# Kernel tuning notes

Measured on AMD Instinct MI355X. Metric: run time of the kernel, lower is better.

## Reference

```python
import jax, jax.numpy as jnp
import numpy as np

B, T, D = 8, 1024, 1024
H, G = 16, 4            # num_heads, query_groups
HD = D // H             # head_dim = 64
REP = H // G            # heads_per_group
EPS = 1e-10
NEG = -1e9


def setup_inputs() -> dict:
    key = jax.random.key(0)
    k1, k2, k3 = jax.random.split(key, 3)
    x = jax.random.normal(k1, (B, T, D), dtype=jnp.float32)
    w_qkv = jax.random.normal(k2, (D, H * HD + 2 * G * HD), dtype=jnp.float32) * (D ** -0.5)
    w_o = jax.random.normal(k3, (D, D), dtype=jnp.float32) * (D ** -0.5)
    padding_mask = jnp.ones((B, T), dtype=bool)
    return {"x": x, "w_qkv": w_qkv, "w_o": w_o, "padding_mask": padding_mask}


def _l2_norm(t):
    # qk_norm_type=2: L2 normalize over head_dim
    return t / (jnp.sqrt(jnp.sum(t * t, axis=-1, keepdims=True)) + EPS)


def reference(x, w_qkv, w_o, padding_mask):
    # fused QKV projection: [B,T,D] @ [D, H*HD + 2*G*HD]
    qkv = x @ w_qkv
    q, k, v = jnp.split(qkv, [H * HD, H * HD + G * HD], axis=-1)
    q = q.reshape(B, T, H, HD)
    k = k.reshape(B, T, G, HD)
    v = v.reshape(B, T, G, HD)
    # QK normalization (L2 over head_dim)
    q = _l2_norm(q)
    k = _l2_norm(k)
    # GQA: expand KV heads (repeat_interleave along head dim)
    k = jnp.repeat(k, REP, axis=2)  # [B,T,H,HD]
    v = jnp.repeat(v, REP, axis=2)
    # to [B,H,T,HD]
    q = q.transpose(0, 2, 1, 3)
    k = k.transpose(0, 2, 1, 3)
    v = v.transpose(0, 2, 1, 3)
    # causal + padding mask, True = attend
    causal = jnp.tril(jnp.ones((T, T), dtype=bool))  # [T_q, T_k]
    valid = padding_mask[:, None, :, None] & padding_mask[:, None, None, :] & causal[None, None]
    scale = HD ** -0.5  # SDPA default scale
    scores = jnp.einsum('bhqd,bhkd->bhqk', q, k) * scale
    scores = jnp.where(valid, scores, NEG)
    attn = jax.nn.softmax(scores, axis=-1)
    out = jnp.einsum('bhqk,bhkd->bhqd', attn, v)  # [B,H,T,HD]
    out = out.transpose(0, 2, 1, 3).reshape(B, T, D)
    return out @ w_o
```

## Files before the change

kernel.cpp:

```cpp
#include <hip/hip_runtime.h>
#include <hip/hip_bf16.h>

typedef __attribute__((ext_vector_type(8))) short short8;
typedef __attribute__((ext_vector_type(4))) short short4v;
typedef __attribute__((ext_vector_type(4))) float f32x4;

#define B_ 8
#define T_ 1024
#define D_ 1024
#define H_ 16
#define G_ 4
#define HD_ 64
#define QKVW 1536

#define GLOAD16(gp, lp) __builtin_amdgcn_global_load_lds( \
    (const __attribute__((address_space(1))) void*)(gp),  \
    (__attribute__((address_space(3))) void*)(lp), 16, 0, 0)

__device__ __forceinline__ float exp2_fast(float x) {
    return __builtin_amdgcn_exp2f(x);
}

__global__ __launch_bounds__(256) void cvt_f32_bf16(
    const float* __restrict__ in, __hip_bfloat16* __restrict__ out, int n)
{
    int i = (blockIdx.x * 256 + threadIdx.x) * 8;
    if (i >= n) return;
    float4 a = *reinterpret_cast<const float4*>(in + i);
    float4 b = *reinterpret_cast<const float4*>(in + i + 4);
    union { short8 s; __hip_bfloat16 h[8]; } u;
    u.h[0] = __float2bfloat16(a.x); u.h[1] = __float2bfloat16(a.y);
    u.h[2] = __float2bfloat16(a.z); u.h[3] = __float2bfloat16(a.w);
    u.h[4] = __float2bfloat16(b.x); u.h[5] = __float2bfloat16(b.y);
    u.h[6] = __float2bfloat16(b.z); u.h[7] = __float2bfloat16(b.w);
    *reinterpret_cast<short8*>(out + i) = u.s;
}

__global__ __launch_bounds__(256) void cvt_transpose(
    const float* __restrict__ in, __hip_bfloat16* __restrict__ outT, int K, int N)
{
    __shared__ float tile[32][33];
    const int k0 = blockIdx.y * 32, n0 = blockIdx.x * 32;
    const int r = threadIdx.x >> 5, c = threadIdx.x & 31;
    #pragma unroll
    for (int i = 0; i < 4; ++i)
        tile[r + i * 8][c] = in[(size_t)(k0 + r + i * 8) * N + n0 + c];
    __syncthreads();
    #pragma unroll
    for (int i = 0; i < 4; ++i)
        outT[(size_t)(n0 + r + i * 8) * K + k0 + c] = __float2bfloat16(tile[c][r + i * 8]);
}

__global__ __launch_bounds__(256) void gemm_qkv(
    const __hip_bfloat16* __restrict__ A,
    const __hip_bfloat16* __restrict__ Bt,
    __hip_bfloat16* __restrict__ qkv,
    __hip_bfloat16* __restrict__ vt)
{
    const int M = B_ * T_, K = D_;
    __shared__ __hip_bfloat16 As[2][128 * 32];
    __shared__ __hip_bfloat16 Bs[2][128 * 32];

    const int tid  = threadIdx.x;
    const int lane = tid & 63;
    const int wr   = (tid >> 6) >> 1;
    const int wc   = (tid >> 6) & 1;

    const int rpx = (M >> 7) >> 3;
    const int xcd = blockIdx.x & 7;
    const int lin = blockIdx.x >> 3;
    const int by  = xcd * rpx + (lin % rpx);
    const int bx  = lin / rpx;
    const int m0 = by * 128;
    const int n0 = bx * 128;

    f32x4 acc[4][4] = {};

    const int s0 = tid * 8,          sr0 = s0 >> 5, sc0 = s0 & 31;
    const int s1 = (256 + tid) * 8,  sr1 = s1 >> 5, sc1 = s1 & 31;

    const __hip_bfloat16* Ar0 = A  + (size_t)(m0 + sr0) * K + sc0;
    const __hip_bfloat16* Ar1 = A  + (size_t)(m0 + sr1) * K + sc1;
    const __hip_bfloat16* Br0 = Bt + (size_t)(n0 + sr0) * K + sc0;
    const __hip_bfloat16* Br1 = Bt + (size_t)(n0 + sr1) * K + sc1;

    const int fr = lane & 15;
    const int kf = (lane >> 4) * 8;

    GLOAD16(Ar0, &As[0][s0]);
    GLOAD16(Ar1, &As[0][s1]);
    GLOAD16(Br0, &Bs[0][s0]);
    GLOAD16(Br1, &Bs[0][s1]);
    __syncthreads();

    int cur = 0;
    for (int kk = 0; kk < K; kk += 32) {
        const int nxt = cur ^ 1;
        if (kk + 32 < K) {
            GLOAD16(Ar0 + kk + 32, &As[nxt][s0]);
            GLOAD16(Ar1 + kk + 32, &As[nxt][s1]);
            GLOAD16(Br0 + kk + 32, &Bs[nxt][s0]);
            GLOAD16(Br1 + kk + 32, &Bs[nxt][s1]);
        }
        short8 a[4], b[4];
        #pragma unroll
        for (int m = 0; m < 4; ++m)
            a[m] = *reinterpret_cast<const short8*>(&As[cur][(wr * 64 + m * 16 + fr) * 32 + kf]);
        #pragma unroll
        for (int n = 0; n < 4; ++n)
            b[n] = *reinterpret_cast<const short8*>(&Bs[cur][(wc * 64 + n * 16 + fr) * 32 + kf]);
        #pragma unroll
        for (int m = 0; m < 4; ++m)
            #pragma unroll
            for (int n = 0; n < 4; ++n)
                acc[m][n] = __builtin_amdgcn_mfma_f32_16x16x32_bf16(a[m], b[n], acc[m][n], 0, 0, 0);
        __syncthreads();
        cur = nxt;
    }

    const int rowb  = m0 + wr * 64 + (lane >> 4) * 4;
    const int colb0 = n0 + wc * 64;

    if (n0 < 1280) {
        const float extra = (n0 < 1024) ? 0.18033688f : 1.0f;
        #pragma unroll
        for (int m = 0; m < 4; ++m)
            #pragma unroll
            for (int r = 0; r < 4; ++r) {
                float ss = 0.f;
                #pragma unroll
                for (int n = 0; n < 4; ++n) { float v = acc[m][n][r]; ss += v * v; }
                ss += __shfl_xor(ss, 1, 64);
                ss += __shfl_xor(ss, 2, 64);
                ss += __shfl_xor(ss, 4, 64);
                ss += __shfl_xor(ss, 8, 64);
                float sc = extra / (sqrtf(ss) + 1e-10f);
                const size_t rbase = (size_t)(rowb + m * 16 + r) * QKVW + colb0 + fr;
                #pragma unroll
                for (int n = 0; n < 4; ++n)
                    qkv[rbase + n * 16] = __float2bfloat16(acc[m][n][r] * sc);
            }
    } else {
        #pragma unroll
        for (int m = 0; m < 4; ++m) {
            const int row = rowb + m * 16;
            const int b   = row >> 10;
            const int t0  = row & 1023;
            #pragma unroll
            for (int n = 0; n < 4; ++n) {
                const int cv = colb0 + fr + n * 16 - 1280;
                const int gg = cv >> 6, d = cv & 63;
                union { short4v s; __hip_bfloat16 h[4]; } u;
                u.h[0] = __float2bfloat16(acc[m][n][0]);
                u.h[1] = __float2bfloat16(acc[m][n][1]);
                u.h[2] = __float2bfloat16(acc[m][n][2]);
                u.h[3] = __float2bfloat16(acc[m][n][3]);
                *reinterpret_cast<short4v*>(
                    vt + ((size_t)((b * G_ + gg) * HD_ + d)) * T_ + t0) = u.s;
            }
        }
    }
}

__global__ __launch_bounds__(256) void gemm_tn_f32(
    const __hip_bfloat16* __restrict__ A,
    const __hip_bfloat16* __restrict__ Bt,
    float* __restrict__ C, int M, int N, int K)
{
    __shared__ __hip_bfloat16 As[2][128 * 32];
    __shared__ __hip_bfloat16 Bs[2][128 * 32];

    const int tid  = threadIdx.x;
    const int lane = tid & 63;
    const int wr   = (tid >> 6) >> 1;
    const int wc   = (tid >> 6) & 1;

    const int rpx = (M >> 7) >> 3;
    const int xcd = blockIdx.x & 7;
    const int lin = blockIdx.x >> 3;
    const int by  = xcd * rpx + (lin % rpx);
    const int bx  = lin / rpx;
    const int m0 = by * 128;
    const int n0 = bx * 128;

    f32x4 acc[4][4] = {};

    const int s0 = tid * 8,          sr0 = s0 >> 5, sc0 = s0 & 31;
    const int s1 = (256 + tid) * 8,  sr1 = s1 >> 5, sc1 = s1 & 31;

    const __hip_bfloat16* Ar0 = A  + (size_t)(m0 + sr0) * K + sc0;
    const __hip_bfloat16* Ar1 = A  + (size_t)(m0 + sr1) * K + sc1;
    const __hip_bfloat16* Br0 = Bt + (size_t)(n0 + sr0) * K + sc0;
    const __hip_bfloat16* Br1 = Bt + (size_t)(n0 + sr1) * K + sc1;

    const int fr = lane & 15;
    const int kf = (lane >> 4) * 8;

    GLOAD16(Ar0, &As[0][s0]);
    GLOAD16(Ar1, &As[0][s1]);
    GLOAD16(Br0, &Bs[0][s0]);
    GLOAD16(Br1, &Bs[0][s1]);
    __syncthreads();

    int cur = 0;
    for (int kk = 0; kk < K; kk += 32) {
        const int nxt = cur ^ 1;
        if (kk + 32 < K) {
            GLOAD16(Ar0 + kk + 32, &As[nxt][s0]);
            GLOAD16(Ar1 + kk + 32, &As[nxt][s1]);
            GLOAD16(Br0 + kk + 32, &Bs[nxt][s0]);
            GLOAD16(Br1 + kk + 32, &Bs[nxt][s1]);
        }
        short8 a[4], b[4];
        #pragma unroll
        for (int m = 0; m < 4; ++m)
            a[m] = *reinterpret_cast<const short8*>(&As[cur][(wr * 64 + m * 16 + fr) * 32 + kf]);
        #pragma unroll
        for (int n = 0; n < 4; ++n)
            b[n] = *reinterpret_cast<const short8*>(&Bs[cur][(wc * 64 + n * 16 + fr) * 32 + kf]);
        #pragma unroll
        for (int m = 0; m < 4; ++m)
            #pragma unroll
            for (int n = 0; n < 4; ++n)
                acc[m][n] = __builtin_amdgcn_mfma_f32_16x16x32_bf16(a[m], b[n], acc[m][n], 0, 0, 0);
        __syncthreads();
        cur = nxt;
    }

    const int rowb = m0 + wr * 64 + (lane >> 4) * 4;
    const int colb = n0 + wc * 64 + fr;
    #pragma unroll
    for (int m = 0; m < 4; ++m)
        #pragma unroll
        for (int n = 0; n < 4; ++n)
            #pragma unroll
            for (int r = 0; r < 4; ++r)
                C[(size_t)(rowb + m * 16 + r) * N + colb + n * 16] = acc[m][n][r];
}

__global__ __launch_bounds__(256) void attn_fwd(
    const __hip_bfloat16* __restrict__ qkv,
    const __hip_bfloat16* __restrict__ vt,
    __hip_bfloat16* __restrict__ out)
{
    const int pair = blockIdx.x;
    const int h  = blockIdx.y;
    const int b  = blockIdx.z;
    const int g  = h >> 2;

    const int tid  = threadIdx.x;
    const int lane = tid & 63;
    const int wid  = tid >> 6;

    __shared__ __hip_bfloat16 Ks[2 * 4096];
    __shared__ __hip_bfloat16 Vs[2 * 4096];
    __shared__ __hip_bfloat16 Ps[4 * 16 * 64];

    const int fr  = lane & 15;
    const int kf  = (lane >> 4) * 8;
    const int kb  = kf * 2;
    const int swz = (fr & 7) << 4;

    const int srow = tid >> 3;
    const int scol = ((tid & 7) * 8) ^ ((srow & 7) << 3);

    const size_t kgbase = (size_t)(b * T_) * QKVW + H_ * HD_ + g * HD_ + scol;
    const size_t vgbase = (size_t)((b * G_ + g) * HD_) * T_ + scol;

    char* PsB = (char*)Ps + wid * 2048;

    for (int half = 0; half < 2; ++half) {
        const int qt = half ? (15 - pair) : pair;
        const int q0 = qt * 64;
        const int arow  = q0 + wid * 16 + fr;
        const int rbase = q0 + wid * 16 + (lane >> 4) * 4;

        short8 qfrag0, qfrag1;
        {
            const size_t qbase = ((size_t)(b * T_ + arow)) * QKVW + h * HD_;
            qfrag0 = *reinterpret_cast<const short8*>(qkv + qbase + kf);
            qfrag1 = *reinterpret_cast<const short8*>(qkv + qbase + 32 + kf);
        }

        float lsum[4] = {0.f, 0.f, 0.f, 0.f};
        f32x4 o[4] = {};

        GLOAD16(qkv + kgbase + (size_t)srow * QKVW,        &Ks[tid * 8]);
        GLOAD16(qkv + kgbase + (size_t)(32 + srow) * QKVW, &Ks[2048 + tid * 8]);
        GLOAD16(vt + vgbase + (size_t)srow * T_,           &Vs[tid * 8]);
        GLOAD16(vt + vgbase + (size_t)(32 + srow) * T_,    &Vs[2048 + tid * 8]);
        __syncthreads();

        int cur = 0;
        for (int kt = 0; kt <= qt; ++kt) {
            const bool diag = (kt == qt);
            const int  nb   = (cur ^ 1) * 4096;

            if (!diag) {
                GLOAD16(qkv + kgbase + (size_t)((kt + 1) * 64 + srow) * QKVW,      &Ks[nb + tid * 8]);
                GLOAD16(qkv + kgbase + (size_t)((kt + 1) * 64 + 32 + srow) * QKVW, &Ks[nb + 2048 + tid * 8]);
                GLOAD16(vt + vgbase + (size_t)srow * T_ + (kt + 1) * 64,           &Vs[nb + tid * 8]);
                GLOAD16(vt + vgbase + (size_t)(32 + srow) * T_ + (kt + 1) * 64,    &Vs[nb + 2048 + tid * 8]);
            }

            char* KsB = (char*)(Ks + cur * 4096);
            char* VsB = (char*)(Vs + cur * 4096);

            f32x4 s[4] = {};
            #pragma unroll
            for (int nf = 0; nf < 4; ++nf) {
                const int row = fr + 16 * nf;
                short8 b0 = *reinterpret_cast<const short8*>(KsB + row * 128 + (kb ^ swz));
                short8 b1 = *reinterpret_cast<const short8*>(KsB + row * 128 + ((64 + kb) ^ swz));
                s[nf] = __builtin_amdgcn_mfma_f32_16x16x32_bf16(qfrag0, b0, s[nf], 0, 0, 0);
                s[nf] = __builtin_amdgcn_mfma_f32_16x16x32_bf16(qfrag1, b1, s[nf], 0, 0, 0);
            }

            if (diag) {
                #pragma unroll
                for (int nf = 0; nf < 4; ++nf) {
                    int col = kt * 64 + fr + 16 * nf;
                    #pragma unroll
                    for (int r = 0; r < 4; ++r) {
                        float p = (col <= rbase + r) ? exp2_fast(s[nf][r]) : 0.f;
                        lsum[r] += p;
                        int q = (lane >> 4) * 4 + r;
                        *(__hip_bfloat16*)(PsB + q * 128 +
                            ((2 * (fr + 16 * nf)) ^ ((q & 7) << 4))) = __float2bfloat16(p);
                    }
                }
            } else {
                #pragma unroll
                for (int nf = 0; nf < 4; ++nf)
                    #pragma unroll
                    for (int r = 0; r < 4; ++r) {
                        float p = exp2_fast(s[nf][r]);
                        lsum[r] += p;
                        int q = (lane >> 4) * 4 + r;
                        *(__hip_bfloat16*)(PsB + q * 128 +
                            ((2 * (fr + 16 * nf)) ^ ((q & 7) << 4))) = __float2bfloat16(p);
                    }
            }

            short8 pa0 = *reinterpret_cast<const short8*>(PsB + fr * 128 + (kb ^ swz));
            short8 pa1 = *reinterpret_cast<const short8*>(PsB + fr * 128 + ((64 + kb) ^ swz));
            #pragma unroll
            for (int nf = 0; nf < 4; ++nf) {
                const int row = fr + 16 * nf;
                short8 b0 = *reinterpret_cast<const short8*>(VsB + row * 128 + (kb ^ swz));
                short8 b1 = *reinterpret_cast<const short8*>(VsB + row * 128 + ((64 + kb) ^ swz));
                o[nf] = __builtin_amdgcn_mfma_f32_16x16x32_bf16(pa0, b0, o[nf], 0, 0, 0);
                o[nf] = __builtin_amdgcn_mfma_f32_16x16x32_bf16(pa1, b1, o[nf], 0, 0, 0);
            }
            __syncthreads();
            cur ^= 1;
        }

        float linv[4];
        #pragma unroll
        for (int r = 0; r < 4; ++r) {
            float v = lsum[r];
            v += __shfl_xor(v, 1, 64);
            v += __shfl_xor(v, 2, 64);
            v += __shfl_xor(v, 4, 64);
            v += __shfl_xor(v, 8, 64);
            linv[r] = 1.0f / v;
        }
        #pragma unroll
        for (int nf = 0; nf < 4; ++nf) {
            int col = fr + 16 * nf;
            #pragma unroll
            for (int r = 0; r < 4; ++r) {
                float v = o[nf][r] * linv[r];
                out[((size_t)(b * T_ + rbase + r)) * (H_ * HD_) + h * HD_ + col] =
                    __float2bfloat16(v);
            }
        }
    }
}

extern "C" void kernel_launch(void* const* d_in, const int* in_sizes, int n_in,
                              void* d_out, int out_size, void* d_ws, size_t ws_size,
                              hipStream_t stream) {
    const float* x_f     = (const float*)d_in[0];
    const float* w_qkv_f = (const float*)d_in[1];
    const float* w_o_f   = (const float*)d_in[2];
    float* out = (float*)d_out;

    const int NX  = B_ * T_ * D_;
    const int NWQ = D_ * QKVW;
    const int NWO = D_ * D_;

    __hip_bfloat16* xb    = (__hip_bfloat16*)d_ws;
    __hip_bfloat16* wqkvT = xb + NX;
    __hip_bfloat16* woT   = wqkvT + NWQ;
    __hip_bfloat16* qkv   = woT + NWO;
    __hip_bfloat16* vt    = qkv + (size_t)(B_ * T_) * QKVW;
    __hip_bfloat16* attn_out = xb;

    dim3 blk(256);

    cvt_f32_bf16<<<dim3(NX / 2048), blk, 0, stream>>>(x_f, xb, NX);
    cvt_transpose<<<dim3(QKVW / 32, D_ / 32), blk, 0, stream>>>(w_qkv_f, wqkvT, D_, QKVW);
    cvt_transpose<<<dim3(D_ / 32, D_ / 32), blk, 0, stream>>>(w_o_f, woT, D_, D_);

    gemm_qkv<<<dim3((QKVW / 128) * ((B_ * T_) / 128)), blk, 0, stream>>>(
        xb, wqkvT, qkv, vt);

    attn_fwd<<<dim3(8, H_, B_), blk, 0, stream>>>(qkv, vt, attn_out);

    gemm_tn_f32<<<dim3((D_ / 128) * ((B_ * T_) / 128)), blk, 0, stream>>>(
        attn_out, woT, out, B_ * T_, D_, D_);
}
```

Measured before the change: 130.3 us.

## Fuse x fp32-to-bf16 conversion into QKV GEMM and interleave attention query tiles

Removes the separate x conversion kernel: the QKV GEMM now loads fp32 x into registers, converts it to bf16 and stores it into LDS after the MFMAs, which saves one full pass over x in global memory. The attention kernel processes its two query tiles (pair and 15-pair) together in a single key loop, so each K/V tile is loaded and read from LDS once for both tiles, and the MFMA sections are wrapped in s_setprio. In exchange the GEMM's A-operand loads go through registers instead of direct-to-LDS loads, and the attention kernel needs more registers and twice the P scratch in LDS, which may lower occupancy.

```diff
diff --git a/kernel.cpp b/kernel.cpp
--- a/kernel.cpp
+++ b/kernel.cpp
@@ -21,19 +21,13 @@
     return __builtin_amdgcn_exp2f(x);
 }
 
-__global__ __launch_bounds__(256) void cvt_f32_bf16(
-    const float* __restrict__ in, __hip_bfloat16* __restrict__ out, int n)
-{
-    int i = (blockIdx.x * 256 + threadIdx.x) * 8;
-    if (i >= n) return;
-    float4 a = *reinterpret_cast<const float4*>(in + i);
-    float4 b = *reinterpret_cast<const float4*>(in + i + 4);
+__device__ __forceinline__ short8 pack_bf16x8(float4 a, float4 b) {
     union { short8 s; __hip_bfloat16 h[8]; } u;
     u.h[0] = __float2bfloat16(a.x); u.h[1] = __float2bfloat16(a.y);
     u.h[2] = __float2bfloat16(a.z); u.h[3] = __float2bfloat16(a.w);
     u.h[4] = __float2bfloat16(b.x); u.h[5] = __float2bfloat16(b.y);
     u.h[6] = __float2bfloat16(b.z); u.h[7] = __float2bfloat16(b.w);
-    *reinterpret_cast<short8*>(out + i) = u.s;
+    return u.s;
 }
 
 __global__ __launch_bounds__(256) void cvt_transpose(
@@ -52,7 +46,7 @@
 }
 
 __global__ __launch_bounds__(256) void gemm_qkv(
-    const __hip_bfloat16* __restrict__ A,
+    const float* __restrict__ Af,
     const __hip_bfloat16* __restrict__ Bt,
     __hip_bfloat16* __restrict__ qkv,
     __hip_bfloat16* __restrict__ vt)
@@ -79,41 +73,52 @@
     const int s0 = tid * 8,          sr0 = s0 >> 5, sc0 = s0 & 31;
     const int s1 = (256 + tid) * 8,  sr1 = s1 >> 5, sc1 = s1 & 31;
 
-    const __hip_bfloat16* Ar0 = A  + (size_t)(m0 + sr0) * K + sc0;
-    const __hip_bfloat16* Ar1 = A  + (size_t)(m0 + sr1) * K + sc1;
+    const float* Ar0f = Af + (size_t)(m0 + sr0) * K + sc0;
+    const float* Ar1f = Af + (size_t)(m0 + sr1) * K + sc1;
     const __hip_bfloat16* Br0 = Bt + (size_t)(n0 + sr0) * K + sc0;
     const __hip_bfloat16* Br1 = Bt + (size_t)(n0 + sr1) * K + sc1;
 
     const int fr = lane & 15;
     const int kf = (lane >> 4) * 8;
 
-    GLOAD16(Ar0, &As[0][s0]);
-    GLOAD16(Ar1, &As[0][s1]);
+    float4 a0a = *(const float4*)(Ar0f);
+    float4 a0b = *(const float4*)(Ar0f + 4);
+    float4 a1a = *(const float4*)(Ar1f);
+    float4 a1b = *(const float4*)(Ar1f + 4);
     GLOAD16(Br0, &Bs[0][s0]);
     GLOAD16(Br1, &Bs[0][s1]);
+    *(short8*)&As[0][s0] = pack_bf16x8(a0a, a0b);
+    *(short8*)&As[0][s1] = pack_bf16x8(a1a, a1b);
     __syncthreads();
 
     int cur = 0;
     for (int kk = 0; kk < K; kk += 32) {
         const int nxt = cur ^ 1;
-        if (kk + 32 < K) {
-            GLOAD16(Ar0 + kk + 32, &As[nxt][s0]);
-            GLOAD16(Ar1 + kk + 32, &As[nxt][s1]);
+        const bool more = (kk + 32 < K);
+        if (more) {
+            a0a = *(const float4*)(Ar0f + kk + 32);
+            a0b = *(const float4*)(Ar0f + kk + 36);
+            a1a = *(const float4*)(Ar1f + kk + 32);
+            a1b = *(const float4*)(Ar1f + kk + 36);
             GLOAD16(Br0 + kk + 32, &Bs[nxt][s0]);
             GLOAD16(Br1 + kk + 32, &Bs[nxt][s1]);
         }
         short8 a[4], b[4];
         #pragma unroll
         for (int m = 0; m < 4; ++m)
-            a[m] = *reinterpret_cast<const short8*>(&As[cur][(wr * 64 + m * 16 + fr) * 32 + kf]);
+            a[m] = *(const short8*)(&As[cur][(wr * 64 + m * 16 + fr) * 32 + kf]);
         #pragma unroll
         for (int n = 0; n < 4; ++n)
-            b[n] = *reinterpret_cast<const short8*>(&Bs[cur][(wc * 64 + n * 16 + fr) * 32 + kf]);
+            b[n] = *(const short8*)(&Bs[cur][(wc * 64 + n * 16 + fr) * 32 + kf]);
         #pragma unroll
         for (int m = 0; m < 4; ++m)
             #pragma unroll
             for (int n = 0; n < 4; ++n)
                 acc[m][n] = __builtin_amdgcn_mfma_f32_16x16x32_bf16(a[m], b[n], acc[m][n], 0, 0, 0);
+        if (more) {
+            *(short8*)&As[nxt][s0] = pack_bf16x8(a0a, a0b);
+            *(short8*)&As[nxt][s1] = pack_bf16x8(a1a, a1b);
+        }
         __syncthreads();
         cur = nxt;
     }
@@ -144,7 +149,7 @@
         #pragma unroll
         for (int m = 0; m < 4; ++m) {
             const int row = rowb + m * 16;
-            const int b   = row >> 10;
+            const int bb  = row >> 10;
             const int t0  = row & 1023;
             #pragma unroll
             for (int n = 0; n < 4; ++n) {
@@ -156,7 +161,7 @@
                 u.h[2] = __float2bfloat16(acc[m][n][2]);
                 u.h[3] = __float2bfloat16(acc[m][n][3]);
                 *reinterpret_cast<short4v*>(
-                    vt + ((size_t)((b * G_ + gg) * HD_ + d)) * T_ + t0) = u.s;
+                    vt + ((size_t)((bb * G_ + gg) * HD_ + d)) * T_ + t0) = u.s;
             }
         }
     }
@@ -214,10 +219,10 @@
         short8 a[4], b[4];
         #pragma unroll
         for (int m = 0; m < 4; ++m)
-            a[m] = *reinterpret_cast<const short8*>(&As[cur][(wr * 64 + m * 16 + fr) * 32 + kf]);
+            a[m] = *(const short8*)(&As[cur][(wr * 64 + m * 16 + fr) * 32 + kf]);
         #pragma unroll
         for (int n = 0; n < 4; ++n)
-            b[n] = *reinterpret_cast<const short8*>(&Bs[cur][(wc * 64 + n * 16 + fr) * 32 + kf]);
+            b[n] = *(const short8*)(&Bs[cur][(wc * 64 + n * 16 + fr) * 32 + kf]);
         #pragma unroll
         for (int m = 0; m < 4; ++m)
             #pragma unroll
@@ -254,7 +259,7 @@
 
     __shared__ __hip_bfloat16 Ks[2 * 4096];
     __shared__ __hip_bfloat16 Vs[2 * 4096];
-    __shared__ __hip_bfloat16 Ps[4 * 16 * 64];
+    __shared__ __hip_bfloat16 Ps[4 * 2 * 1024];
 
     const int fr  = lane & 15;
     const int kf  = (lane >> 4) * 8;
@@ -267,63 +272,78 @@
     const size_t kgbase = (size_t)(b * T_) * QKVW + H_ * HD_ + g * HD_ + scol;
     const size_t vgbase = (size_t)((b * G_ + g) * HD_) * T_ + scol;
 
-    char* PsB = (char*)Ps + wid * 2048;
-
-    for (int half = 0; half < 2; ++half) {
-        const int qt = half ? (15 - pair) : pair;
-        const int q0 = qt * 64;
-        const int arow  = q0 + wid * 16 + fr;
-        const int rbase = q0 + wid * 16 + (lane >> 4) * 4;
-
-        short8 qfrag0, qfrag1;
-        {
-            const size_t qbase = ((size_t)(b * T_ + arow)) * QKVW + h * HD_;
-            qfrag0 = *reinterpret_cast<const short8*>(qkv + qbase + kf);
-            qfrag1 = *reinterpret_cast<const short8*>(qkv + qbase + 32 + kf);
-        }
-
-        float lsum[4] = {0.f, 0.f, 0.f, 0.f};
-        f32x4 o[4] = {};
-
-        GLOAD16(qkv + kgbase + (size_t)srow * QKVW,        &Ks[tid * 8]);
-        GLOAD16(qkv + kgbase + (size_t)(32 + srow) * QKVW, &Ks[2048 + tid * 8]);
-        GLOAD16(vt + vgbase + (size_t)srow * T_,           &Vs[tid * 8]);
-        GLOAD16(vt + vgbase + (size_t)(32 + srow) * T_,    &Vs[2048 + tid * 8]);
-        __syncthreads();
-
-        int cur = 0;
-        for (int kt = 0; kt <= qt; ++kt) {
-            const bool diag = (kt == qt);
-            const int  nb   = (cur ^ 1) * 4096;
-
-            if (!diag) {
-                GLOAD16(qkv + kgbase + (size_t)((kt + 1) * 64 + srow) * QKVW,      &Ks[nb + tid * 8]);
-                GLOAD16(qkv + kgbase + (size_t)((kt + 1) * 64 + 32 + srow) * QKVW, &Ks[nb + 2048 + tid * 8]);
-                GLOAD16(vt + vgbase + (size_t)srow * T_ + (kt + 1) * 64,           &Vs[nb + tid * 8]);
-                GLOAD16(vt + vgbase + (size_t)(32 + srow) * T_ + (kt + 1) * 64,    &Vs[nb + 2048 + tid * 8]);
-            }
-
-            char* KsB = (char*)(Ks + cur * 4096);
-            char* VsB = (char*)(Vs + cur * 4096);
-
-            f32x4 s[4] = {};
+    char* PsB = (char*)Ps + wid * 4096;
+
+    const int qtA = pair, qtB = 15 - pair;
+    const int rbaseA = qtA * 64 + wid * 16 + (lane >> 4) * 4;
+    const int rbaseB = qtB * 64 + wid * 16 + (lane >> 4) * 4;
+
+    short8 qA0, qA1, qB0, qB1;
+    {
+        const size_t qa = ((size_t)(b * T_ + qtA * 64 + wid * 16 + fr)) * QKVW + h * HD_;
+        const size_t qb = ((size_t)(b * T_ + qtB * 64 + wid * 16 + fr)) * QKVW + h * HD_;
+        qA0 = *(const short8*)(qkv + qa + kf);
+        qA1 = *(const short8*)(qkv + qa + 32 + kf);
+        qB0 = *(const short8*)(qkv + qb + kf);
+        qB1 = *(const short8*)(qkv + qb + 32 + kf);
+    }
+
+    float lsumA[4] = {0.f, 0.f, 0.f, 0.f}, lsumB[4] = {0.f, 0.f, 0.f, 0.f};
+    f32x4 oA[4] = {}, oB[4] = {};
+
+    GLOAD16(qkv + kgbase + (size_t)srow * QKVW,        &Ks[tid * 8]);
+    GLOAD16(qkv + kgbase + (size_t)(32 + srow) * QKVW, &Ks[2048 + tid * 8]);
+    GLOAD16(vt + vgbase + (size_t)srow * T_,           &Vs[tid * 8]);
+    GLOAD16(vt + vgbase + (size_t)(32 + srow) * T_,    &Vs[2048 + tid * 8]);
+    __syncthreads();
+
+    int cur = 0;
+    for (int kt = 0; kt <= qtB; ++kt) {
+        const bool doA = (kt <= qtA);
+        const int nb = (cur ^ 1) * 4096;
+        if (kt < qtB) {
+            GLOAD16(qkv + kgbase + (size_t)((kt + 1) * 64 + srow) * QKVW,      &Ks[nb + tid * 8]);
+            GLOAD16(qkv + kgbase + (size_t)((kt + 1) * 64 + 32 + srow) * QKVW, &Ks[nb + 2048 + tid * 8]);
+            GLOAD16(vt + vgbase + (size_t)srow * T_ + (kt + 1) * 64,           &Vs[nb + tid * 8]);
+            GLOAD16(vt + vgbase + (size_t)(32 + srow) * T_ + (kt + 1) * 64,    &Vs[nb + 2048 + tid * 8]);
+        }
+
+        char* KsB = (char*)(Ks + cur * 4096);
+        char* VsB = (char*)(Vs + cur * 4096);
+
+        short8 bK0[4], bK1[4];
+        #pragma unroll
+        for (int nf = 0; nf < 4; ++nf) {
+            const int row = fr + 16 * nf;
+            bK0[nf] = *(const short8*)(KsB + row * 128 + (kb ^ swz));
+            bK1[nf] = *(const short8*)(KsB + row * 128 + ((64 + kb) ^ swz));
+        }
+
+        f32x4 sA[4] = {}, sB[4] = {};
+        __builtin_amdgcn_s_setprio(1);
+        if (doA) {
             #pragma unroll
             for (int nf = 0; nf < 4; ++nf) {
-                const int row = fr + 16 * nf;
-                short8 b0 = *reinterpret_cast<const short8*>(KsB + row * 128 + (kb ^ swz));
-                short8 b1 = *reinterpret_cast<const short8*>(KsB + row * 128 + ((64 + kb) ^ swz));
-                s[nf] = __builtin_amdgcn_mfma_f32_16x16x32_bf16(qfrag0, b0, s[nf], 0, 0, 0);
-                s[nf] = __builtin_amdgcn_mfma_f32_16x16x32_bf16(qfrag1, b1, s[nf], 0, 0, 0);
-            }
-
-            if (diag) {
+                sA[nf] = __builtin_amdgcn_mfma_f32_16x16x32_bf16(qA0, bK0[nf], sA[nf], 0, 0, 0);
+                sA[nf] = __builtin_amdgcn_mfma_f32_16x16x32_bf16(qA1, bK1[nf], sA[nf], 0, 0, 0);
+            }
+        }
+        #pragma unroll
+        for (int nf = 0; nf < 4; ++nf) {
+            sB[nf] = __builtin_amdgcn_mfma_f32_16x16x32_bf16(qB0, bK0[nf], sB[nf], 0, 0, 0);
+            sB[nf] = __builtin_amdgcn_mfma_f32_16x16x32_bf16(qB1, bK1[nf], sB[nf], 0, 0, 0);
+        }
+        __builtin_amdgcn_s_setprio(0);
+
+        if (doA) {
+            if (kt == qtA) {
                 #pragma unroll
                 for (int nf = 0; nf < 4; ++nf) {
                     int col = kt * 64 + fr + 16 * nf;
                     #pragma unroll
                     for (int r = 0; r < 4; ++r) {
-                        float p = (col <= rbase + r) ? exp2_fast(s[nf][r]) : 0.f;
-                        lsum[r] += p;
+                        float p = (col <= rbaseA + r) ? exp2_fast(sA[nf][r]) : 0.f;
+                        lsumA[r] += p;
                         int q = (lane >> 4) * 4 + r;
                         *(__hip_bfloat16*)(PsB + q * 128 +
                             ((2 * (fr + 16 * nf)) ^ ((q & 7) << 4))) = __float2bfloat16(p);
@@ -334,47 +354,96 @@
                 for (int nf = 0; nf < 4; ++nf)
                     #pragma unroll
                     for (int r = 0; r < 4; ++r) {
-                        float p = exp2_fast(s[nf][r]);
-                        lsum[r] += p;
+                        float p = exp2_fast(sA[nf][r]);
+                        lsumA[r] += p;
                         int q = (lane >> 4) * 4 + r;
                         *(__hip_bfloat16*)(PsB + q * 128 +
                             ((2 * (fr + 16 * nf)) ^ ((q & 7) << 4))) = __float2bfloat16(p);
                     }
             }
-
-            short8 pa0 = *reinterpret_cast<const short8*>(PsB + fr * 128 + (kb ^ swz));
-            short8 pa1 = *reinterpret_cast<const short8*>(PsB + fr * 128 + ((64 + kb) ^ swz));
+        }
+        if (kt == qtB) {
             #pragma unroll
             for (int nf = 0; nf < 4; ++nf) {
-                const int row = fr + 16 * nf;
-                short8 b0 = *reinterpret_cast<const short8*>(VsB + row * 128 + (kb ^ swz));
-                short8 b1 = *reinterpret_cast<const short8*>(VsB + row * 128 + ((64 + kb) ^ swz));
-                o[nf] = __builtin_amdgcn_mfma_f32_16x16x32_bf16(pa0, b0, o[nf], 0, 0, 0);
-                o[nf] = __builtin_amdgcn_mfma_f32_16x16x32_bf16(pa1, b1, o[nf], 0, 0, 0);
-            }
-            __syncthreads();
-            cur ^= 1;
-        }
-
-        float linv[4];
+                int col = kt * 64 + fr + 16 * nf;
+                #pragma unroll
+                for (int r = 0; r < 4; ++r) {
+                    float p = (col <= rbaseB + r) ? exp2_fast(sB[nf][r]) : 0.f;
+                    lsumB[r] += p;
+                    int q = (lane >> 4) * 4 + r;
+                    *(__hip_bfloat16*)(PsB + 2048 + q * 128 +
+                        ((2 * (fr + 16 * nf)) ^ ((q & 7) << 4))) = __float2bfloat16(p);
+                }
+            }
+        } else {
+            #pragma unroll
+            for (int nf = 0; nf < 4; ++nf)
+                #pragma unroll
+                for (int r = 0; r < 4; ++r) {
+                    float p = exp2_fast(sB[nf][r]);
+                    lsumB[r] += p;
+                    int q = (lane >> 4) * 4 + r;
+                    *(__hip_bfloat16*)(PsB + 2048 + q * 128 +
+                        ((2 * (fr + 16 * nf)) ^ ((q & 7) << 4))) = __float2bfloat16(p);
+                }
+        }
+
+        short8 bV0[4], bV1[4];
+        #pragma unroll
+        for (int nf = 0; nf < 4; ++nf) {
+            const int row = fr + 16 * nf;
+            bV0[nf] = *(const short8*)(VsB + row * 128 + (kb ^ swz));
+            bV1[nf] = *(const short8*)(VsB + row * 128 + ((64 + kb) ^ swz));
+        }
+        __builtin_amdgcn_s_setprio(1);
+        if (doA) {
+            short8 pa0 = *(const short8*)(PsB + fr * 128 + (kb ^ swz));
+            short8 pa1 = *(const short8*)(PsB + fr * 128 + ((64 + kb) ^ swz));
+            #pragma unroll
+            for (int nf = 0; nf < 4; ++nf) {
+                oA[nf] = __builtin_amdgcn_mfma_f32_16x16x32_bf16(pa0, bV0[nf], oA[nf], 0, 0, 0);
+                oA[nf] = __builtin_amdgcn_mfma_f32_16x16x32_bf16(pa1, bV1[nf], oA[nf], 0, 0, 0);
+            }
+        }
+        {
+            short8 pb0 = *(const short8*)(PsB + 2048 + fr * 128 + (kb ^ swz));
+            short8 pb1 = *(const short8*)(PsB + 2048 + fr * 128 + ((64 + kb) ^ swz));
+            #pragma unroll
+            for (int nf = 0; nf < 4; ++nf) {
+                oB[nf] = __builtin_amdgcn_mfma_f32_16x16x32_bf16(pb0, bV0[nf], oB[nf], 0, 0, 0);
+                oB[nf] = __builtin_amdgcn_mfma_f32_16x16x32_bf16(pb1, bV1[nf], oB[nf], 0, 0, 0);
+            }
+        }
+        __builtin_amdgcn_s_setprio(0);
+        __syncthreads();
+        cur ^= 1;
+    }
+
+    float linvA[4], linvB[4];
+    #pragma unroll
+    for (int r = 0; r < 4; ++r) {
+        float va = lsumA[r];
+        va += __shfl_xor(va, 1, 64);
+        va += __shfl_xor(va, 2, 64);
+        va += __shfl_xor(va, 4, 64);
+        va += __shfl_xor(va, 8, 64);
+        linvA[r] = 1.0f / va;
+        float vb = lsumB[r];
+        vb += __shfl_xor(vb, 1, 64);
+        vb += __shfl_xor(vb, 2, 64);
+        vb += __shfl_xor(vb, 4, 64);
+        vb += __shfl_xor(vb, 8, 64);
+        linvB[r] = 1.0f / vb;
+    }
+    #pragma unroll
+    for (int nf = 0; nf < 4; ++nf) {
+        int col = fr + 16 * nf;
         #pragma unroll
         for (int r = 0; r < 4; ++r) {
-            float v = lsum[r];
-            v += __shfl_xor(v, 1, 64);
-            v += __shfl_xor(v, 2, 64);
-            v += __shfl_xor(v, 4, 64);
-            v += __shfl_xor(v, 8, 64);
-            linv[r] = 1.0f / v;
-        }
-        #pragma unroll
-        for (int nf = 0; nf < 4; ++nf) {
-            int col = fr + 16 * nf;
-            #pragma unroll
-            for (int r = 0; r < 4; ++r) {
-                float v = o[nf][r] * linv[r];
-                out[((size_t)(b * T_ + rbase + r)) * (H_ * HD_) + h * HD_ + col] =
-                    __float2bfloat16(v);
-            }
+            out[((size_t)(b * T_ + rbaseA + r)) * (H_ * HD_) + h * HD_ + col] =
+                __float2bfloat16(oA[nf][r] * linvA[r]);
+            out[((size_t)(b * T_ + rbaseB + r)) * (H_ * HD_) + h * HD_ + col] =
+                __float2bfloat16(oB[nf][r] * linvB[r]);
         }
     }
 }
@@ -391,21 +460,19 @@
     const int NWQ = D_ * QKVW;
     const int NWO = D_ * D_;
 
-    __hip_bfloat16* xb    = (__hip_bfloat16*)d_ws;
-    __hip_bfloat16* wqkvT = xb + NX;
+    __hip_bfloat16* attn_out = (__hip_bfloat16*)d_ws;
+    __hip_bfloat16* wqkvT = attn_out + NX;
     __hip_bfloat16* woT   = wqkvT + NWQ;
     __hip_bfloat16* qkv   = woT + NWO;
     __hip_bfloat16* vt    = qkv + (size_t)(B_ * T_) * QKVW;
-    __hip_bfloat16* attn_out = xb;
 
     dim3 blk(256);
 
-    cvt_f32_bf16<<<dim3(NX / 2048), blk, 0, stream>>>(x_f, xb, NX);
     cvt_transpose<<<dim3(QKVW / 32, D_ / 32), blk, 0, stream>>>(w_qkv_f, wqkvT, D_, QKVW);
     cvt_transpose<<<dim3(D_ / 32, D_ / 32), blk, 0, stream>>>(w_o_f, woT, D_, D_);
 
     gemm_qkv<<<dim3((QKVW / 128) * ((B_ * T_) / 128)), blk, 0, stream>>>(
-        xb, wqkvT, qkv, vt);
+        x_f, wqkvT, qkv, vt);
 
     attn_fwd<<<dim3(8, H_, B_), blk, 0, stream>>>(qkv, vt, attn_out);
 
```

Measured after the change: 129.9 us. No clear change (-0.3%).

## Fuse x conversion into QKV GEMM and split attention into per-tile blocks

Applied to the files above, without the earlier changes.

The QKV GEMM now reads fp32 x directly, holds the next tile in registers and converts it to bf16 into LDS after the MFMAs, which removes the separate conversion kernel and its bf16 round trip through memory. The attention kernel no longer pairs query tiles (qt and 15-qt) in one block; it launches 16 blocks per head with one query tile each and adds s_setprio around the MFMA sections. The fused load path adds register pressure and synchronous global loads inside the GEMM loop. The unpaired attention grid gives blocks very different causal workloads and relies on the scheduler to balance them.

```diff
diff --git a/kernel.cpp b/kernel.cpp
--- a/kernel.cpp
+++ b/kernel.cpp
@@ -21,19 +21,13 @@
     return __builtin_amdgcn_exp2f(x);
 }
 
-__global__ __launch_bounds__(256) void cvt_f32_bf16(
-    const float* __restrict__ in, __hip_bfloat16* __restrict__ out, int n)
-{
-    int i = (blockIdx.x * 256 + threadIdx.x) * 8;
-    if (i >= n) return;
-    float4 a = *reinterpret_cast<const float4*>(in + i);
-    float4 b = *reinterpret_cast<const float4*>(in + i + 4);
+__device__ __forceinline__ short8 pack_bf16x8(float4 a, float4 b) {
     union { short8 s; __hip_bfloat16 h[8]; } u;
     u.h[0] = __float2bfloat16(a.x); u.h[1] = __float2bfloat16(a.y);
     u.h[2] = __float2bfloat16(a.z); u.h[3] = __float2bfloat16(a.w);
     u.h[4] = __float2bfloat16(b.x); u.h[5] = __float2bfloat16(b.y);
     u.h[6] = __float2bfloat16(b.z); u.h[7] = __float2bfloat16(b.w);
-    *reinterpret_cast<short8*>(out + i) = u.s;
+    return u.s;
 }
 
 __global__ __launch_bounds__(256) void cvt_transpose(
@@ -52,7 +46,7 @@
 }
 
 __global__ __launch_bounds__(256) void gemm_qkv(
-    const __hip_bfloat16* __restrict__ A,
+    const float* __restrict__ Af,
     const __hip_bfloat16* __restrict__ Bt,
     __hip_bfloat16* __restrict__ qkv,
     __hip_bfloat16* __restrict__ vt)
@@ -79,41 +73,52 @@
     const int s0 = tid * 8,          sr0 = s0 >> 5, sc0 = s0 & 31;
     const int s1 = (256 + tid) * 8,  sr1 = s1 >> 5, sc1 = s1 & 31;
 
-    const __hip_bfloat16* Ar0 = A  + (size_t)(m0 + sr0) * K + sc0;
-    const __hip_bfloat16* Ar1 = A  + (size_t)(m0 + sr1) * K + sc1;
+    const float* Ar0f = Af + (size_t)(m0 + sr0) * K + sc0;
+    const float* Ar1f = Af + (size_t)(m0 + sr1) * K + sc1;
     const __hip_bfloat16* Br0 = Bt + (size_t)(n0 + sr0) * K + sc0;
     const __hip_bfloat16* Br1 = Bt + (size_t)(n0 + sr1) * K + sc1;
 
     const int fr = lane & 15;
     const int kf = (lane >> 4) * 8;
 
-    GLOAD16(Ar0, &As[0][s0]);
-    GLOAD16(Ar1, &As[0][s1]);
+    float4 a0a = *(const float4*)(Ar0f);
+    float4 a0b = *(const float4*)(Ar0f + 4);
+    float4 a1a = *(const float4*)(Ar1f);
+    float4 a1b = *(const float4*)(Ar1f + 4);
     GLOAD16(Br0, &Bs[0][s0]);
     GLOAD16(Br1, &Bs[0][s1]);
+    *(short8*)&As[0][s0] = pack_bf16x8(a0a, a0b);
+    *(short8*)&As[0][s1] = pack_bf16x8(a1a, a1b);
     __syncthreads();
 
     int cur = 0;
     for (int kk = 0; kk < K; kk += 32) {
         const int nxt = cur ^ 1;
-        if (kk + 32 < K) {
-            GLOAD16(Ar0 + kk + 32, &As[nxt][s0]);
-            GLOAD16(Ar1 + kk + 32, &As[nxt][s1]);
+        const bool more = (kk + 32 < K);
+        if (more) {
+            a0a = *(const float4*)(Ar0f + kk + 32);
+            a0b = *(const float4*)(Ar0f + kk + 36);
+            a1a = *(const float4*)(Ar1f + kk + 32);
+            a1b = *(const float4*)(Ar1f + kk + 36);
             GLOAD16(Br0 + kk + 32, &Bs[nxt][s0]);
             GLOAD16(Br1 + kk + 32, &Bs[nxt][s1]);
         }
         short8 a[4], b[4];
         #pragma unroll
         for (int m = 0; m < 4; ++m)
-            a[m] = *reinterpret_cast<const short8*>(&As[cur][(wr * 64 + m * 16 + fr) * 32 + kf]);
+            a[m] = *(const short8*)(&As[cur][(wr * 64 + m * 16 + fr) * 32 + kf]);
         #pragma unroll
         for (int n = 0; n < 4; ++n)
-            b[n] = *reinterpret_cast<const short8*>(&Bs[cur][(wc * 64 + n * 16 + fr) * 32 + kf]);
+            b[n] = *(const short8*)(&Bs[cur][(wc * 64 + n * 16 + fr) * 32 + kf]);
         #pragma unroll
         for (int m = 0; m < 4; ++m)
             #pragma unroll
             for (int n = 0; n < 4; ++n)
                 acc[m][n] = __builtin_amdgcn_mfma_f32_16x16x32_bf16(a[m], b[n], acc[m][n], 0, 0, 0);
+        if (more) {
+            *(short8*)&As[nxt][s0] = pack_bf16x8(a0a, a0b);
+            *(short8*)&As[nxt][s1] = pack_bf16x8(a1a, a1b);
+        }
         __syncthreads();
         cur = nxt;
     }
@@ -144,7 +149,7 @@
         #pragma unroll
         for (int m = 0; m < 4; ++m) {
             const int row = rowb + m * 16;
-            const int b   = row >> 10;
+            const int bb  = row >> 10;
             const int t0  = row & 1023;
             #pragma unroll
             for (int n = 0; n < 4; ++n) {
@@ -156,7 +161,7 @@
                 u.h[2] = __float2bfloat16(acc[m][n][2]);
                 u.h[3] = __float2bfloat16(acc[m][n][3]);
                 *reinterpret_cast<short4v*>(
-                    vt + ((size_t)((b * G_ + gg) * HD_ + d)) * T_ + t0) = u.s;
+                    vt + ((size_t)((bb * G_ + gg) * HD_ + d)) * T_ + t0) = u.s;
             }
         }
     }
@@ -214,10 +219,10 @@
         short8 a[4], b[4];
         #pragma unroll
         for (int m = 0; m < 4; ++m)
-            a[m] = *reinterpret_cast<const short8*>(&As[cur][(wr * 64 + m * 16 + fr) * 32 + kf]);
+            a[m] = *(const short8*)(&As[cur][(wr * 64 + m * 16 + fr) * 32 + kf]);
         #pragma unroll
         for (int n = 0; n < 4; ++n)
-            b[n] = *reinterpret_cast<const short8*>(&Bs[cur][(wc * 64 + n * 16 + fr) * 32 + kf]);
+            b[n] = *(const short8*)(&Bs[cur][(wc * 64 + n * 16 + fr) * 32 + kf]);
         #pragma unroll
         for (int m = 0; m < 4; ++m)
             #pragma unroll
@@ -243,7 +248,7 @@
     const __hip_bfloat16* __restrict__ vt,
     __hip_bfloat16* __restrict__ out)
 {
-    const int pair = blockIdx.x;
+    const int qt = blockIdx.x;
     const int h  = blockIdx.y;
     const int b  = blockIdx.z;
     const int g  = h >> 2;
@@ -254,7 +259,7 @@
 
     __shared__ __hip_bfloat16 Ks[2 * 4096];
     __shared__ __hip_bfloat16 Vs[2 * 4096];
-    __shared__ __hip_bfloat16 Ps[4 * 16 * 64];
+    __shared__ __hip_bfloat16 Ps[4 * 1024];
 
     const int fr  = lane & 15;
     const int kf  = (lane >> 4) * 8;
@@ -269,112 +274,113 @@
 
     char* PsB = (char*)Ps + wid * 2048;
 
-    for (int half = 0; half < 2; ++half) {
-        const int qt = half ? (15 - pair) : pair;
-        const int q0 = qt * 64;
-        const int arow  = q0 + wid * 16 + fr;
-        const int rbase = q0 + wid * 16 + (lane >> 4) * 4;
-
-        short8 qfrag0, qfrag1;
-        {
-            const size_t qbase = ((size_t)(b * T_ + arow)) * QKVW + h * HD_;
-            qfrag0 = *reinterpret_cast<const short8*>(qkv + qbase + kf);
-            qfrag1 = *reinterpret_cast<const short8*>(qkv + qbase + 32 + kf);
-        }
-
-        float lsum[4] = {0.f, 0.f, 0.f, 0.f};
-        f32x4 o[4] = {};
-
-        GLOAD16(qkv + kgbase + (size_t)srow * QKVW,        &Ks[tid * 8]);
-        GLOAD16(qkv + kgbase + (size_t)(32 + srow) * QKVW, &Ks[2048 + tid * 8]);
-        GLOAD16(vt + vgbase + (size_t)srow * T_,           &Vs[tid * 8]);
-        GLOAD16(vt + vgbase + (size_t)(32 + srow) * T_,    &Vs[2048 + tid * 8]);
+    const int q0 = qt * 64;
+    const int arow  = q0 + wid * 16 + fr;
+    const int rbase = q0 + wid * 16 + (lane >> 4) * 4;
+
+    short8 qfrag0, qfrag1;
+    {
+        const size_t qbase = ((size_t)(b * T_ + arow)) * QKVW + h * HD_;
+        qfrag0 = *(const short8*)(qkv + qbase + kf);
+        qfrag1 = *(const short8*)(qkv + qbase + 32 + kf);
+    }
+
+    float lsum[4] = {0.f, 0.f, 0.f, 0.f};
+    f32x4 o[4] = {};
+
+    GLOAD16(qkv + kgbase + (size_t)srow * QKVW,        &Ks[tid * 8]);
+    GLOAD16(qkv + kgbase + (size_t)(32 + srow) * QKVW, &Ks[2048 + tid * 8]);
+    GLOAD16(vt + vgbase + (size_t)srow * T_,           &Vs[tid * 8]);
+    GLOAD16(vt + vgbase + (size_t)(32 + srow) * T_,    &Vs[2048 + tid * 8]);
+    __syncthreads();
+
+    int cur = 0;
+    for (int kt = 0; kt <= qt; ++kt) {
+        const bool diag = (kt == qt);
+        const int  nb   = (cur ^ 1) * 4096;
+
+        if (!diag) {
+            GLOAD16(qkv + kgbase + (size_t)((kt + 1) * 64 + srow) * QKVW,      &Ks[nb + tid * 8]);
+            GLOAD16(qkv + kgbase + (size_t)((kt + 1) * 64 + 32 + srow) * QKVW, &Ks[nb + 2048 + tid * 8]);
+            GLOAD16(vt + vgbase + (size_t)srow * T_ + (kt + 1) * 64,           &Vs[nb + tid * 8]);
+            GLOAD16(vt + vgbase + (size_t)(32 + srow) * T_ + (kt + 1) * 64,    &Vs[nb + 2048 + tid * 8]);
+        }
+
+        char* KsB = (char*)(Ks + cur * 4096);
+        char* VsB = (char*)(Vs + cur * 4096);
+
+        f32x4 s[4] = {};
+        __builtin_amdgcn_s_setprio(1);
+        #pragma unroll
+        for (int nf = 0; nf < 4; ++nf) {
+            const int row = fr + 16 * nf;
+            short8 b0 = *(const short8*)(KsB + row * 128 + (kb ^ swz));
+            short8 b1 = *(const short8*)(KsB + row * 128 + ((64 + kb) ^ swz));
+            s[nf] = __builtin_amdgcn_mfma_f32_16x16x32_bf16(qfrag0, b0, s[nf], 0, 0, 0);
+            s[nf] = __builtin_amdgcn_mfma_f32_16x16x32_bf16(qfrag1, b1, s[nf], 0, 0, 0);
+        }
+        __builtin_amdgcn_s_setprio(0);
+
+        if (diag) {
+            #pragma unroll
+            for (int nf = 0; nf < 4; ++nf) {
+                int col = kt * 64 + fr + 16 * nf;
+                #pragma unroll
+                for (int r = 0; r < 4; ++r) {
+                    float p = (col <= rbase + r) ? exp2_fast(s[nf][r]) : 0.f;
+                    lsum[r] += p;
+                    int q = (lane >> 4) * 4 + r;
+                    *(__hip_bfloat16*)(PsB + q * 128 +
+                        ((2 * (fr + 16 * nf)) ^ ((q & 7) << 4))) = __float2bfloat16(p);
+                }
+            }
+        } else {
+            #pragma unroll
+            for (int nf = 0; nf < 4; ++nf)
+                #pragma unroll
+                for (int r = 0; r < 4; ++r) {
+                    float p = exp2_fast(s[nf][r]);
+                    lsum[r] += p;
+                    int q = (lane >> 4) * 4 + r;
+                    *(__hip_bfloat16*)(PsB + q * 128 +
+                        ((2 * (fr + 16 * nf)) ^ ((q & 7) << 4))) = __float2bfloat16(p);
+                }
+        }
+
+        short8 pa0 = *(const short8*)(PsB + fr * 128 + (kb ^ swz));
+        short8 pa1 = *(const short8*)(PsB + fr * 128 + ((64 + kb) ^ swz));
+        __builtin_amdgcn_s_setprio(1);
+        #pragma unroll
+        for (int nf = 0; nf < 4; ++nf) {
+            const int row = fr + 16 * nf;
+            short8 b0 = *(const short8*)(VsB + row * 128 + (kb ^ swz));
+            short8 b1 = *(const short8*)(VsB + row * 128 + ((64 + kb) ^ swz));
+            o[nf] = __builtin_amdgcn_mfma_f32_16x16x32_bf16(pa0, b0, o[nf], 0, 0, 0);
+            o[nf] = __builtin_amdgcn_mfma_f32_16x16x32_bf16(pa1, b1, o[nf], 0, 0, 0);
+        }
+        __builtin_amdgcn_s_setprio(0);
         __syncthreads();
-
-        int cur = 0;
-        for (int kt = 0; kt <= qt; ++kt) {
-            const bool diag = (kt == qt);
-            const int  nb   = (cur ^ 1) * 4096;
-
-            if (!diag) {
-                GLOAD16(qkv + kgbase + (size_t)((kt + 1) * 64 + srow) * QKVW,      &Ks[nb + tid * 8]);
-                GLOAD16(qkv + kgbase + (size_t)((kt + 1) * 64 + 32 + srow) * QKVW, &Ks[nb + 2048 + tid * 8]);
-                GLOAD16(vt + vgbase + (size_t)srow * T_ + (kt + 1) * 64,           &Vs[nb + tid * 8]);
-                GLOAD16(vt + vgbase + (size_t)(32 + srow) * T_ + (kt + 1) * 64,    &Vs[nb + 2048 + tid * 8]);
-            }
-
-            char* KsB = (char*)(Ks + cur * 4096);
-            char* VsB = (char*)(Vs + cur * 4096);
-
-            f32x4 s[4] = {};
-            #pragma unroll
-            for (int nf = 0; nf < 4; ++nf) {
-                const int row = fr + 16 * nf;
-                short8 b0 = *reinterpret_cast<const short8*>(KsB + row * 128 + (kb ^ swz));
-                short8 b1 = *reinterpret_cast<const short8*>(KsB + row * 128 + ((64 + kb) ^ swz));
-                s[nf] = __builtin_amdgcn_mfma_f32_16x16x32_bf16(qfrag0, b0, s[nf], 0, 0, 0);
-                s[nf] = __builtin_amdgcn_mfma_f32_16x16x32_bf16(qfrag1, b1, s[nf], 0, 0, 0);
-            }
-
-            if (diag) {
-                #pragma unroll
-                for (int nf = 0; nf < 4; ++nf) {
-                    int col = kt * 64 + fr + 16 * nf;
-                    #pragma unroll
-                    for (int r = 0; r < 4; ++r) {
-                        float p = (col <= rbase + r) ? exp2_fast(s[nf][r]) : 0.f;
-                        lsum[r] += p;
-                        int q = (lane >> 4) * 4 + r;
-                        *(__hip_bfloat16*)(PsB + q * 128 +
-                            ((2 * (fr + 16 * nf)) ^ ((q & 7) << 4))) = __float2bfloat16(p);
-                    }
-                }
-            } else {
-                #pragma unroll
-                for (int nf = 0; nf < 4; ++nf)
-                    #pragma unroll
-                    for (int r = 0; r < 4; ++r) {
-                        float p = exp2_fast(s[nf][r]);
-                        lsum[r] += p;
-                        int q = (lane >> 4) * 4 + r;
-                        *(__hip_bfloat16*)(PsB + q * 128 +
-                            ((2 * (fr + 16 * nf)) ^ ((q & 7) << 4))) = __float2bfloat16(p);
-                    }
-            }
-
-            short8 pa0 = *reinterpret_cast<const short8*>(PsB + fr * 128 + (kb ^ swz));
-            short8 pa1 = *reinterpret_cast<const short8*>(PsB + fr * 128 + ((64 + kb) ^ swz));
-            #pragma unroll
-            for (int nf = 0; nf < 4; ++nf) {
-                const int row = fr + 16 * nf;
-                short8 b0 = *reinterpret_cast<const short8*>(VsB + row * 128 + (kb ^ swz));
-                short8 b1 = *reinterpret_cast<const short8*>(VsB + row * 128 + ((64 + kb) ^ swz));
-                o[nf] = __builtin_amdgcn_mfma_f32_16x16x32_bf16(pa0, b0, o[nf], 0, 0, 0);
-                o[nf] = __builtin_amdgcn_mfma_f32_16x16x32_bf16(pa1, b1, o[nf], 0, 0, 0);
-            }
-            __syncthreads();
-            cur ^= 1;
-        }
-
-        float linv[4];
+        cur ^= 1;
+    }
+
+    float linv[4];
+    #pragma unroll
+    for (int r = 0; r < 4; ++r) {
+        float v = lsum[r];
+        v += __shfl_xor(v, 1, 64);
+        v += __shfl_xor(v, 2, 64);
+        v += __shfl_xor(v, 4, 64);
+        v += __shfl_xor(v, 8, 64);
+        linv[r] = 1.0f / v;
+    }
+    #pragma unroll
+    for (int nf = 0; nf < 4; ++nf) {
+        int col = fr + 16 * nf;
         #pragma unroll
         for (int r = 0; r < 4; ++r) {
-            float v = lsum[r];
-            v += __shfl_xor(v, 1, 64);
-            v += __shfl_xor(v, 2, 64);
-            v += __shfl_xor(v, 4, 64);
-            v += __shfl_xor(v, 8, 64);
-            linv[r] = 1.0f / v;
-        }
-        #pragma unroll
-        for (int nf = 0; nf < 4; ++nf) {
-            int col = fr + 16 * nf;
-            #pragma unroll
-            for (int r = 0; r < 4; ++r) {
-                float v = o[nf][r] * linv[r];
-                out[((size_t)(b * T_ + rbase + r)) * (H_ * HD_) + h * HD_ + col] =
-                    __float2bfloat16(v);
-            }
+            float v = o[nf][r] * linv[r];
+            out[((size_t)(b * T_ + rbase + r)) * (H_ * HD_) + h * HD_ + col] =
+                __float2bfloat16(v);
         }
     }
 }
@@ -391,23 +397,21 @@
     const int NWQ = D_ * QKVW;
     const int NWO = D_ * D_;
 
-    __hip_bfloat16* xb    = (__hip_bfloat16*)d_ws;
-    __hip_bfloat16* wqkvT = xb + NX;
+    __hip_bfloat16* attn_out = (__hip_bfloat16*)d_ws;
+    __hip_bfloat16* wqkvT = attn_out + NX;
     __hip_bfloat16* woT   = wqkvT + NWQ;
     __hip_bfloat16* qkv   = woT + NWO;
     __hip_bfloat16* vt    = qkv + (size_t)(B_ * T_) * QKVW;
-    __hip_bfloat16* attn_out = xb;
 
     dim3 blk(256);
 
-    cvt_f32_bf16<<<dim3(NX / 2048), blk, 0, stream>>>(x_f, xb, NX);
     cvt_transpose<<<dim3(QKVW / 32, D_ / 32), blk, 0, stream>>>(w_qkv_f, wqkvT, D_, QKVW);
     cvt_transpose<<<dim3(D_ / 32, D_ / 32), blk, 0, stream>>>(w_o_f, woT, D_, D_);
 
     gemm_qkv<<<dim3((QKVW / 128) * ((B_ * T_) / 128)), blk, 0, stream>>>(
-        xb, wqkvT, qkv, vt);
-
-    attn_fwd<<<dim3(8, H_, B_), blk, 0, stream>>>(qkv, vt, attn_out);
+        x_f, wqkvT, qkv, vt);
+
+    attn_fwd<<<dim3(16, H_, B_), blk, 0, stream>>>(qkv, vt, attn_out);
 
     gemm_tn_f32<<<dim3((D_ / 128) * ((B_ * T_) / 128)), blk, 0, stream>>>(
         attn_out, woT, out, B_ * T_, D_, D_);
```

Result: slower. 140.6 us (+7.9%).
